# Optimization experiments

Hardware: AMD Instinct MI355X
Metric: run time of the kernel (lower is better)

The kernel has to match this reference:

```python
import jax, jax.numpy as jnp
import numpy as np

GROUP = 64  # quantization group size along the input dim


def dequantize(W_q, scale, zero):
    """int4 dequant: W_q uint8-packed [out, in/2] (two nibbles per byte),
    group-wise affine scale/zero [out, in/GROUP]. Returns float [out, in]."""
    out, half = W_q.shape
    hi = (W_q >> 4) & 0xF
    lo = W_q & 0xF
    w = jnp.stack([hi, lo], axis=-1).reshape(out, half * 2).astype(scale.dtype)
    w = w.reshape(out, -1, GROUP)  # [out, n_groups, GROUP]
    w = (w - zero[:, :, None]) * scale[:, :, None]
    return w.reshape(out, half * 2)


def setup_inputs() -> dict:
    key = jax.random.key(0)
    ks = jax.random.split(key, 10)
    hidden, inter = 4096, 11008
    B, S = 4, 1024
    x = jax.random.normal(ks[0], (B, S, hidden), dtype=jnp.float32)
    gate_Wq = jax.random.randint(ks[1], (inter, hidden // 2), 0, 256, dtype=jnp.int32)
    up_Wq = jax.random.randint(ks[2], (inter, hidden // 2), 0, 256, dtype=jnp.int32)
    down_Wq = jax.random.randint(ks[3], (hidden, inter // 2), 0, 256, dtype=jnp.int32)
    # small scales keep activations sane; zero points in [0, 15]
    gate_scale = jax.random.uniform(ks[4], (inter, hidden // GROUP)) * 0.01 + 1e-4
    gate_zero = jax.random.uniform(ks[5], (inter, hidden // GROUP)) * 15.0
    up_scale = jax.random.uniform(ks[6], (inter, hidden // GROUP)) * 0.01 + 1e-4
    up_zero = jax.random.uniform(ks[7], (inter, hidden // GROUP)) * 15.0
    down_scale = jax.random.uniform(ks[8], (hidden, inter // GROUP)) * 0.01 + 1e-4
    down_zero = jax.random.uniform(ks[9], (hidden, inter // GROUP)) * 15.0
    return {"x": x, "gate_Wq": gate_Wq, "up_Wq": up_Wq, "down_Wq": down_Wq,
            "gate_scale": gate_scale, "gate_zero": gate_zero,
            "up_scale": up_scale, "up_zero": up_zero,
            "down_scale": down_scale, "down_zero": down_zero}


def reference(x, gate_Wq, up_Wq, down_Wq, gate_scale, gate_zero,
              up_scale, up_zero, down_scale, down_zero):
    Wg = dequantize(gate_Wq, gate_scale, gate_zero)  # [inter, hidden]
    Wu = dequantize(up_Wq, up_scale, up_zero)        # [inter, hidden]
    Wd = dequantize(down_Wq, down_scale, down_zero)  # [hidden, inter]
    g = jnp.einsum('bsh,ih->bsi', x, Wg)
    u = jnp.einsum('bsh,ih->bsi', x, Wu)
    h = jax.nn.silu(g) * u
    return jnp.einsum('bsi,hi->bsh', h, Wd)
```

## Files before the change

### kernel.cpp

```cpp
#include <hip/hip_runtime.h>
#include <hip/hip_fp16.h>
#include <cstdint>
#include <cstddef>

#define HIDDEN 4096
#define INTER  11008
#define NTOK   4096
#define NG1    (HIDDEN/64)
#define NG2    (INTER/64)

typedef _Float16 f16;
typedef _Float16 f16x8 __attribute__((ext_vector_type(8)));
typedef float    f32x4 __attribute__((ext_vector_type(4)));

__device__ __forceinline__ void g2lds16(const void* g, void* l) {
  __builtin_amdgcn_global_load_lds(
      (const __attribute__((address_space(1))) uint32_t*)g,
      (__attribute__((address_space(3))) uint32_t*)l, 16, 0, 0);
}

__device__ __forceinline__ uint32_t dq2(uint32_t b, __half2 s2, __half2 nzs) {
  uint32_t qb = 0x64006400u | (b >> 4) | ((b & 0xFu) << 16);
  __half2 hq = __builtin_bit_cast(__half2, qb);
  __half2 t  = __hsub2(hq, __builtin_bit_cast(__half2, 0x64006400u));
  __half2 wv = __hfma2(t, s2, nzs);
  return __builtin_bit_cast(uint32_t, wv);
}

__global__ __launch_bounds__(256) void cvt_x(const float* __restrict__ x,
                                             f16* __restrict__ xh) {
  size_t i = ((size_t)blockIdx.x * 256 + threadIdx.x) * 8;
  float4 a = *(const float4*)(x + i);
  float4 b = *(const float4*)(x + i + 4);
  f16x8 o = {(f16)a.x, (f16)a.y, (f16)a.z, (f16)a.w,
             (f16)b.x, (f16)b.y, (f16)b.z, (f16)b.w};
  *(f16x8*)(xh + i) = o;
}

__global__ __launch_bounds__(512, 4) void gemm_gateup(
    const f16* __restrict__ xh,
    const uint32_t* __restrict__ gq, const uint32_t* __restrict__ uq,
    const float* __restrict__ gs, const float* __restrict__ gz,
    const float* __restrict__ us, const float* __restrict__ uz,
    f16* __restrict__ h) {
  extern __shared__ char smem[];
  f16* lA0 = (f16*)smem;
  f16* lA1 = (f16*)(smem + 32768);
  char* lBg = smem + 65536;
  char* lBu = smem + 73728;
  const int tid = threadIdx.x, lane = tid & 63, wave = tid >> 6;
  const int bm = blockIdx.x, bn = blockIdx.y;
  const int wm = wave >> 1, wn = wave & 1;

  const int arow0 = tid >> 3;
  const int ak8s  = (tid & 7) ^ (arow0 & 7);
  const f16* aptr = xh + (size_t)(bm * 256 + arow0) * HIDDEN + ak8s * 8;
  const int aoff = tid * 16;

  const int mat = tid >> 8;
  const int t = tid & 255;
  const int brow0 = t >> 3;
  const uint32_t* qp = (mat ? uq : gq) + (size_t)(bn * 64 + brow0) * (HIDDEN / 2) + (t & 7) * 4;
  const float* sp = (mat ? us : gs) + (size_t)(bn * 64 + brow0) * NG1;
  const float* zp = (mat ? uz : gz) + (size_t)(bn * 64 + brow0) * NG1;
  char* lb = mat ? lBu : lBg;
  const int bws0 = brow0 * 128 + (((t & 7) ^ (brow0 & 7)) << 4);

  int abase[4], asel[4];
#pragma unroll
  for (int im = 0; im < 4; ++im) {
    int r = wm * 64 + im * 16 + (lane & 15);
    abase[im] = r * 128; asel[im] = r & 7;
  }
  int bbase[2], bsel[2];
#pragma unroll
  for (int in_ = 0; in_ < 2; ++in_) {
    int r = wn * 32 + in_ * 16 + (lane & 15);
    bbase[in_] = r * 128; bsel[in_] = r & 7;
  }
  const int kchunk = lane >> 4;

  f32x4 accg[4][2] = {};
  f32x4 accu[4][2] = {};

  auto stageA = [&](const f16* src, f16* dst) {
#pragma unroll
    for (int i = 0; i < 4; ++i)
      g2lds16(src + (size_t)i * 64 * HIDDEN, (char*)dst + aoff + i * 8192);
  };
  auto loadB = [&](int ktn, uint4& w0, uint4& w1,
                   float& s0f, float& z0f, float& s1f, float& z1f) {
    w0 = *(const uint4*)(qp + (size_t)ktn * 32);
    w1 = *(const uint4*)(qp + (size_t)32 * (HIDDEN / 2) + (size_t)ktn * 32);
    s0f = sp[ktn]; z0f = zp[ktn];
    s1f = sp[32 * NG1 + ktn]; z1f = zp[32 * NG1 + ktn];
  };
  auto writeB = [&](uint4 w0, uint4 w1, float s0f, float z0f, float s1f, float z1f) {
    __half2 s0 = __float2half2_rn(s0f), n0 = __float2half2_rn(-z0f * s0f);
    __half2 s1 = __float2half2_rn(s1f), n1 = __float2half2_rn(-z1f * s1f);
    uint4 o0, o1;
    o0.x = dq2(w0.x, s0, n0); o0.y = dq2(w0.y, s0, n0);
    o0.z = dq2(w0.z, s0, n0); o0.w = dq2(w0.w, s0, n0);
    o1.x = dq2(w1.x, s1, n1); o1.y = dq2(w1.y, s1, n1);
    o1.z = dq2(w1.z, s1, n1); o1.w = dq2(w1.w, s1, n1);
    *(uint4*)(lb + bws0) = o0;
    *(uint4*)(lb + bws0 + 32 * 128) = o1;
  };
  auto compute = [&](const f16* lA) {
#pragma unroll
    for (int ks = 0; ks < 2; ++ks) {
      int kc = ks * 4 + kchunk;
      f16x8 a[4], bg[2], bu[2];
#pragma unroll
      for (int im = 0; im < 4; ++im)
        a[im] = *(const f16x8*)((const char*)lA + abase[im] + ((kc ^ asel[im]) << 4));
#pragma unroll
      for (int in_ = 0; in_ < 2; ++in_) {
        bg[in_] = *(const f16x8*)(lBg + bbase[in_] + ((kc ^ bsel[in_]) << 4));
        bu[in_] = *(const f16x8*)(lBu + bbase[in_] + ((kc ^ bsel[in_]) << 4));
      }
#pragma unroll
      for (int im = 0; im < 4; ++im)
#pragma unroll
        for (int in_ = 0; in_ < 2; ++in_) {
          accg[im][in_] = __builtin_amdgcn_mfma_f32_16x16x32_f16(a[im], bg[in_], accg[im][in_], 0, 0, 0);
          accu[im][in_] = __builtin_amdgcn_mfma_f32_16x16x32_f16(a[im], bu[in_], accu[im][in_], 0, 0, 0);
        }
    }
  };

  stageA(aptr, lA0);
  {
    uint4 w0, w1; float s0f, z0f, s1f, z1f;
    loadB(0, w0, w1, s0f, z0f, s1f, z1f);
    writeB(w0, w1, s0f, z0f, s1f, z1f);
  }
  __syncthreads();

  for (int kt = 0; kt < NG1 - 1; ++kt) {
    stageA(aptr + (size_t)(kt + 1) * 64, (kt & 1) ? lA0 : lA1);
    uint4 w0, w1; float s0f, z0f, s1f, z1f;
    loadB(kt + 1, w0, w1, s0f, z0f, s1f, z1f);
    compute((kt & 1) ? lA1 : lA0);
    __syncthreads();
    writeB(w0, w1, s0f, z0f, s1f, z1f);
    __syncthreads();
  }
  compute(((NG1 - 1) & 1) ? lA1 : lA0);

#pragma unroll
  for (int im = 0; im < 4; ++im)
#pragma unroll
    for (int in_ = 0; in_ < 2; ++in_)
#pragma unroll
      for (int r = 0; r < 4; ++r) {
        int row = bm * 256 + wm * 64 + im * 16 + (lane >> 4) * 4 + r;
        int col = bn * 64 + wn * 32 + in_ * 16 + (lane & 15);
        float g = accg[im][in_][r];
        float u = accu[im][in_][r];
        float hv = (g / (1.0f + __expf(-g))) * u;
        h[(size_t)row * INTER + col] = (f16)hv;
      }
}

__global__ __launch_bounds__(512, 4) void gemm_down(
    const f16* __restrict__ h, const uint32_t* __restrict__ dq_,
    const float* __restrict__ dsc, const float* __restrict__ dz,
    float* __restrict__ out) {
  extern __shared__ char smem[];
  f16* lA0 = (f16*)smem;
  f16* lA1 = (f16*)(smem + 32768);
  char* lB = smem + 65536;
  const int tid = threadIdx.x, lane = tid & 63, wave = tid >> 6;
  const int bm = blockIdx.x, bn = blockIdx.y;
  const int wm = wave >> 1, wn = wave & 1;

  const int arow0 = tid >> 3;
  const int ak8s  = (tid & 7) ^ (arow0 & 7);
  const f16* aptr = h + (size_t)(bm * 256 + arow0) * INTER + ak8s * 8;
  const int aoff = tid * 16;

  const int brow0 = tid >> 3;
  const uint32_t* qp = dq_ + (size_t)(bn * 128 + brow0) * (INTER / 2) + (tid & 7) * 4;
  const float* sp = dsc + (size_t)(bn * 128 + brow0) * NG2;
  const float* zp = dz + (size_t)(bn * 128 + brow0) * NG2;
  const int bws0 = brow0 * 128 + (((tid & 7) ^ (brow0 & 7)) << 4);

  int abase[4], asel[4];
#pragma unroll
  for (int im = 0; im < 4; ++im) {
    int r = wm * 64 + im * 16 + (lane & 15);
    abase[im] = r * 128; asel[im] = r & 7;
  }
  int bbase[4], bsel[4];
#pragma unroll
  for (int in_ = 0; in_ < 4; ++in_) {
    int r = wn * 64 + in_ * 16 + (lane & 15);
    bbase[in_] = r * 128; bsel[in_] = r & 7;
  }
  const int kchunk = lane >> 4;

  f32x4 acc[4][4] = {};

  auto stageA = [&](const f16* src, f16* dst) {
#pragma unroll
    for (int i = 0; i < 4; ++i)
      g2lds16(src + (size_t)i * 64 * INTER, (char*)dst + aoff + i * 8192);
  };
  auto loadB = [&](int ktn, uint4& w0, uint4& w1,
                   float& s0f, float& z0f, float& s1f, float& z1f) {
    w0 = *(const uint4*)(qp + (size_t)ktn * 32);
    w1 = *(const uint4*)(qp + (size_t)64 * (INTER / 2) + (size_t)ktn * 32);
    s0f = sp[ktn]; z0f = zp[ktn];
    s1f = sp[64 * NG2 + ktn]; z1f = zp[64 * NG2 + ktn];
  };
  auto writeB = [&](uint4 w0, uint4 w1, float s0f, float z0f, float s1f, float z1f) {
    __half2 s0 = __float2half2_rn(s0f), n0 = __float2half2_rn(-z0f * s0f);
    __half2 s1 = __float2half2_rn(s1f), n1 = __float2half2_rn(-z1f * s1f);
    uint4 o0, o1;
    o0.x = dq2(w0.x, s0, n0); o0.y = dq2(w0.y, s0, n0);
    o0.z = dq2(w0.z, s0, n0); o0.w = dq2(w0.w, s0, n0);
    o1.x = dq2(w1.x, s1, n1); o1.y = dq2(w1.y, s1, n1);
    o1.z = dq2(w1.z, s1, n1); o1.w = dq2(w1.w, s1, n1);
    *(uint4*)(lB + bws0) = o0;
    *(uint4*)(lB + bws0 + 64 * 128) = o1;
  };
  auto compute = [&](const f16* lA) {
#pragma unroll
    for (int ks = 0; ks < 2; ++ks) {
      int kc = ks * 4 + kchunk;
      f16x8 a[4], b[4];
#pragma unroll
      for (int im = 0; im < 4; ++im)
        a[im] = *(const f16x8*)((const char*)lA + abase[im] + ((kc ^ asel[im]) << 4));
#pragma unroll
      for (int in_ = 0; in_ < 4; ++in_)
        b[in_] = *(const f16x8*)(lB + bbase[in_] + ((kc ^ bsel[in_]) << 4));
#pragma unroll
      for (int im = 0; im < 4; ++im)
#pragma unroll
        for (int in_ = 0; in_ < 4; ++in_)
          acc[im][in_] = __builtin_amdgcn_mfma_f32_16x16x32_f16(a[im], b[in_], acc[im][in_], 0, 0, 0);
    }
  };

  stageA(aptr, lA0);
  {
    uint4 w0, w1; float s0f, z0f, s1f, z1f;
    loadB(0, w0, w1, s0f, z0f, s1f, z1f);
    writeB(w0, w1, s0f, z0f, s1f, z1f);
  }
  __syncthreads();

  for (int kt = 0; kt < NG2 - 1; ++kt) {
    stageA(aptr + (size_t)(kt + 1) * 64, (kt & 1) ? lA0 : lA1);
    uint4 w0, w1; float s0f, z0f, s1f, z1f;
    loadB(kt + 1, w0, w1, s0f, z0f, s1f, z1f);
    compute((kt & 1) ? lA1 : lA0);
    __syncthreads();
    writeB(w0, w1, s0f, z0f, s1f, z1f);
    __syncthreads();
  }
  compute(((NG2 - 1) & 1) ? lA1 : lA0);

#pragma unroll
  for (int im = 0; im < 4; ++im)
#pragma unroll
    for (int in_ = 0; in_ < 4; ++in_)
#pragma unroll
      for (int r = 0; r < 4; ++r) {
        int row = bm * 256 + wm * 64 + im * 16 + (lane >> 4) * 4 + r;
        int col = bn * 128 + wn * 64 + in_ * 16 + (lane & 15);
        out[(size_t)row * HIDDEN + col] = acc[im][in_][r];
      }
}

extern "C" void kernel_launch(void* const* d_in, const int* in_sizes, int n_in,
                              void* d_out, int out_size, void* d_ws, size_t ws_size,
                              hipStream_t stream) {
  const float*    x   = (const float*)d_in[0];
  const uint32_t* gq  = (const uint32_t*)d_in[1];
  const uint32_t* uq  = (const uint32_t*)d_in[2];
  const uint32_t* dqw = (const uint32_t*)d_in[3];
  const float*    gs  = (const float*)d_in[4];
  const float*    gz  = (const float*)d_in[5];
  const float*    us  = (const float*)d_in[6];
  const float*    uz  = (const float*)d_in[7];
  const float*    dsc = (const float*)d_in[8];
  const float*    dzz = (const float*)d_in[9];

  f16* xh   = (f16*)d_ws;
  f16* hbuf = (f16*)((char*)d_ws + (size_t)NTOK * HIDDEN * 2);
  float* out = (float*)d_out;

  const int LDS_BYTES = 80 * 1024;
  (void)hipFuncSetAttribute((const void*)gemm_gateup,
                            hipFuncAttributeMaxDynamicSharedMemorySize, LDS_BYTES);
  (void)hipFuncSetAttribute((const void*)gemm_down,
                            hipFuncAttributeMaxDynamicSharedMemorySize, LDS_BYTES);

  cvt_x<<<dim3((NTOK * HIDDEN) / (256 * 8)), 256, 0, stream>>>(x, xh);
  gemm_gateup<<<dim3(NTOK / 256, INTER / 64), 512, LDS_BYTES, stream>>>(
      xh, gq, uq, gs, gz, us, uz, hbuf);
  gemm_down<<<dim3(NTOK / 256, HIDDEN / 128), 512, LDS_BYTES, stream>>>(
      hbuf, dqw, dsc, dzz, out);
}
```

Baseline: 1.502 ms.

## Register-prefetch A and B, double-buffer dequantized B in LDS, prioritize MFMA

Replaces direct global-to-LDS A staging with register loads written into a single LDS A buffer, and double-buffers the dequantized B tile so the next tile's dequant write overlaps the current compute. Raw B data is prefetched two steps ahead, MFMA sections are raised with s_setprio, and barriers wait only on LDS counters. LDS drops to 64KB. The cost is more VGPR pressure and exposed global-load latency before the A write.

```diff
diff --git a/kernel.cpp b/kernel.cpp
--- a/kernel.cpp
+++ b/kernel.cpp
@@ -13,10 +13,10 @@
 typedef _Float16 f16x8 __attribute__((ext_vector_type(8)));
 typedef float    f32x4 __attribute__((ext_vector_type(4)));
 
-__device__ __forceinline__ void g2lds16(const void* g, void* l) {
-  __builtin_amdgcn_global_load_lds(
-      (const __attribute__((address_space(1))) uint32_t*)g,
-      (__attribute__((address_space(3))) uint32_t*)l, 16, 0, 0);
+__device__ __forceinline__ void wg_barrier_lgkm() {
+  asm volatile("s_waitcnt lgkmcnt(0)" ::: "memory");
+  __builtin_amdgcn_s_barrier();
+  asm volatile("" ::: "memory");
 }
 
 __device__ __forceinline__ uint32_t dq2(uint32_t b, __half2 s2, __half2 nzs) {
@@ -26,6 +26,8 @@
   __half2 wv = __hfma2(t, s2, nzs);
   return __builtin_bit_cast(uint32_t, wv);
 }
+
+struct Bp { uint4 w0, w1; float s0, z0, s1, z1; };
 
 __global__ __launch_bounds__(256) void cvt_x(const float* __restrict__ x,
                                              f16* __restrict__ xh) {
@@ -44,10 +46,9 @@
     const float* __restrict__ us, const float* __restrict__ uz,
     f16* __restrict__ h) {
   extern __shared__ char smem[];
-  f16* lA0 = (f16*)smem;
-  f16* lA1 = (f16*)(smem + 32768);
-  char* lBg = smem + 65536;
-  char* lBu = smem + 73728;
+  f16* lA = (f16*)smem;
+  char* lBgBase = smem + 32768;
+  char* lBuBase = smem + 49152;
   const int tid = threadIdx.x, lane = tid & 63, wave = tid >> 6;
   const int bm = blockIdx.x, bn = blockIdx.y;
   const int wm = wave >> 1, wn = wave & 1;
@@ -63,7 +64,7 @@
   const uint32_t* qp = (mat ? uq : gq) + (size_t)(bn * 64 + brow0) * (HIDDEN / 2) + (t & 7) * 4;
   const float* sp = (mat ? us : gs) + (size_t)(bn * 64 + brow0) * NG1;
   const float* zp = (mat ? uz : gz) + (size_t)(bn * 64 + brow0) * NG1;
-  char* lb = mat ? lBu : lBg;
+  char* lbBase = mat ? lBuBase : lBgBase;
   const int bws0 = brow0 * 128 + (((t & 7) ^ (brow0 & 7)) << 4);
 
   int abase[4], asel[4];
@@ -83,30 +84,38 @@
   f32x4 accg[4][2] = {};
   f32x4 accu[4][2] = {};
 
-  auto stageA = [&](const f16* src, f16* dst) {
+  uint4 ar[4];
+  auto loadA = [&](int kt) {
 #pragma unroll
     for (int i = 0; i < 4; ++i)
-      g2lds16(src + (size_t)i * 64 * HIDDEN, (char*)dst + aoff + i * 8192);
-  };
-  auto loadB = [&](int ktn, uint4& w0, uint4& w1,
-                   float& s0f, float& z0f, float& s1f, float& z1f) {
-    w0 = *(const uint4*)(qp + (size_t)ktn * 32);
-    w1 = *(const uint4*)(qp + (size_t)32 * (HIDDEN / 2) + (size_t)ktn * 32);
-    s0f = sp[ktn]; z0f = zp[ktn];
-    s1f = sp[32 * NG1 + ktn]; z1f = zp[32 * NG1 + ktn];
-  };
-  auto writeB = [&](uint4 w0, uint4 w1, float s0f, float z0f, float s1f, float z1f) {
-    __half2 s0 = __float2half2_rn(s0f), n0 = __float2half2_rn(-z0f * s0f);
-    __half2 s1 = __float2half2_rn(s1f), n1 = __float2half2_rn(-z1f * s1f);
+      ar[i] = *(const uint4*)(aptr + (size_t)kt * 64 + (size_t)i * 64 * HIDDEN);
+  };
+  auto writeA = [&]() {
+#pragma unroll
+    for (int i = 0; i < 4; ++i)
+      *(uint4*)((char*)lA + aoff + i * 8192) = ar[i];
+  };
+  auto loadB = [&](int ktn, Bp& r) {
+    r.w0 = *(const uint4*)(qp + (size_t)ktn * 32);
+    r.w1 = *(const uint4*)(qp + (size_t)32 * (HIDDEN / 2) + (size_t)ktn * 32);
+    r.s0 = sp[ktn]; r.z0 = zp[ktn];
+    r.s1 = sp[32 * NG1 + ktn]; r.z1 = zp[32 * NG1 + ktn];
+  };
+  auto writeB = [&](const Bp& r, int pb) {
+    char* lb = lbBase + pb * 8192;
+    __half2 s0 = __float2half2_rn(r.s0), n0 = __float2half2_rn(-r.z0 * r.s0);
+    __half2 s1 = __float2half2_rn(r.s1), n1 = __float2half2_rn(-r.z1 * r.s1);
     uint4 o0, o1;
-    o0.x = dq2(w0.x, s0, n0); o0.y = dq2(w0.y, s0, n0);
-    o0.z = dq2(w0.z, s0, n0); o0.w = dq2(w0.w, s0, n0);
-    o1.x = dq2(w1.x, s1, n1); o1.y = dq2(w1.y, s1, n1);
-    o1.z = dq2(w1.z, s1, n1); o1.w = dq2(w1.w, s1, n1);
+    o0.x = dq2(r.w0.x, s0, n0); o0.y = dq2(r.w0.y, s0, n0);
+    o0.z = dq2(r.w0.z, s0, n0); o0.w = dq2(r.w0.w, s0, n0);
+    o1.x = dq2(r.w1.x, s1, n1); o1.y = dq2(r.w1.y, s1, n1);
+    o1.z = dq2(r.w1.z, s1, n1); o1.w = dq2(r.w1.w, s1, n1);
     *(uint4*)(lb + bws0) = o0;
     *(uint4*)(lb + bws0 + 32 * 128) = o1;
   };
-  auto compute = [&](const f16* lA) {
+  auto compute = [&](int cb) {
+    const char* bg0 = lBgBase + cb * 8192;
+    const char* bu0 = lBuBase + cb * 8192;
 #pragma unroll
     for (int ks = 0; ks < 2; ++ks) {
       int kc = ks * 4 + kchunk;
@@ -116,9 +125,10 @@
         a[im] = *(const f16x8*)((const char*)lA + abase[im] + ((kc ^ asel[im]) << 4));
 #pragma unroll
       for (int in_ = 0; in_ < 2; ++in_) {
-        bg[in_] = *(const f16x8*)(lBg + bbase[in_] + ((kc ^ bsel[in_]) << 4));
-        bu[in_] = *(const f16x8*)(lBu + bbase[in_] + ((kc ^ bsel[in_]) << 4));
+        bg[in_] = *(const f16x8*)(bg0 + bbase[in_] + ((kc ^ bsel[in_]) << 4));
+        bu[in_] = *(const f16x8*)(bu0 + bbase[in_] + ((kc ^ bsel[in_]) << 4));
       }
+      __builtin_amdgcn_s_setprio(1);
 #pragma unroll
       for (int im = 0; im < 4; ++im)
 #pragma unroll
@@ -126,27 +136,30 @@
           accg[im][in_] = __builtin_amdgcn_mfma_f32_16x16x32_f16(a[im], bg[in_], accg[im][in_], 0, 0, 0);
           accu[im][in_] = __builtin_amdgcn_mfma_f32_16x16x32_f16(a[im], bu[in_], accu[im][in_], 0, 0, 0);
         }
+      __builtin_amdgcn_s_setprio(0);
     }
   };
 
-  stageA(aptr, lA0);
-  {
-    uint4 w0, w1; float s0f, z0f, s1f, z1f;
-    loadB(0, w0, w1, s0f, z0f, s1f, z1f);
-    writeB(w0, w1, s0f, z0f, s1f, z1f);
-  }
-  __syncthreads();
+  loadA(0);
+  Bp br0, brc, brn;
+  loadB(0, br0);
+  loadB(1, brc);
+  writeA();
+  writeB(br0, 0);
+  wg_barrier_lgkm();
 
   for (int kt = 0; kt < NG1 - 1; ++kt) {
-    stageA(aptr + (size_t)(kt + 1) * 64, (kt & 1) ? lA0 : lA1);
-    uint4 w0, w1; float s0f, z0f, s1f, z1f;
-    loadB(kt + 1, w0, w1, s0f, z0f, s1f, z1f);
-    compute((kt & 1) ? lA1 : lA0);
-    __syncthreads();
-    writeB(w0, w1, s0f, z0f, s1f, z1f);
-    __syncthreads();
-  }
-  compute(((NG1 - 1) & 1) ? lA1 : lA0);
+    loadA(kt + 1);
+    loadB(kt + 2 < NG1 ? kt + 2 : NG1 - 1, brn);
+    __builtin_amdgcn_sched_barrier(0);
+    writeB(brc, (kt + 1) & 1);
+    compute(kt & 1);
+    wg_barrier_lgkm();
+    writeA();
+    wg_barrier_lgkm();
+    brc = brn;
+  }
+  compute((NG1 - 1) & 1);
 
 #pragma unroll
   for (int im = 0; im < 4; ++im)
@@ -168,9 +181,8 @@
     const float* __restrict__ dsc, const float* __restrict__ dz,
     float* __restrict__ out) {
   extern __shared__ char smem[];
-  f16* lA0 = (f16*)smem;
-  f16* lA1 = (f16*)(smem + 32768);
-  char* lB = smem + 65536;
+  f16* lA = (f16*)smem;
+  char* lBBase = smem + 32768;
   const int tid = threadIdx.x, lane = tid & 63, wave = tid >> 6;
   const int bm = blockIdx.x, bn = blockIdx.y;
   const int wm = wave >> 1, wn = wave & 1;
@@ -202,30 +214,37 @@
 
   f32x4 acc[4][4] = {};
 
-  auto stageA = [&](const f16* src, f16* dst) {
+  uint4 ar[4];
+  auto loadA = [&](int kt) {
 #pragma unroll
     for (int i = 0; i < 4; ++i)
-      g2lds16(src + (size_t)i * 64 * INTER, (char*)dst + aoff + i * 8192);
-  };
-  auto loadB = [&](int ktn, uint4& w0, uint4& w1,
-                   float& s0f, float& z0f, float& s1f, float& z1f) {
-    w0 = *(const uint4*)(qp + (size_t)ktn * 32);
-    w1 = *(const uint4*)(qp + (size_t)64 * (INTER / 2) + (size_t)ktn * 32);
-    s0f = sp[ktn]; z0f = zp[ktn];
-    s1f = sp[64 * NG2 + ktn]; z1f = zp[64 * NG2 + ktn];
-  };
-  auto writeB = [&](uint4 w0, uint4 w1, float s0f, float z0f, float s1f, float z1f) {
-    __half2 s0 = __float2half2_rn(s0f), n0 = __float2half2_rn(-z0f * s0f);
-    __half2 s1 = __float2half2_rn(s1f), n1 = __float2half2_rn(-z1f * s1f);
+      ar[i] = *(const uint4*)(aptr + (size_t)kt * 64 + (size_t)i * 64 * INTER);
+  };
+  auto writeA = [&]() {
+#pragma unroll
+    for (int i = 0; i < 4; ++i)
+      *(uint4*)((char*)lA + aoff + i * 8192) = ar[i];
+  };
+  auto loadB = [&](int ktn, Bp& r) {
+    r.w0 = *(const uint4*)(qp + (size_t)ktn * 32);
+    r.w1 = *(const uint4*)(qp + (size_t)64 * (INTER / 2) + (size_t)ktn * 32);
+    r.s0 = sp[ktn]; r.z0 = zp[ktn];
+    r.s1 = sp[64 * NG2 + ktn]; r.z1 = zp[64 * NG2 + ktn];
+  };
+  auto writeB = [&](const Bp& r, int pb) {
+    char* lb = lBBase + pb * 16384;
+    __half2 s0 = __float2half2_rn(r.s0), n0 = __float2half2_rn(-r.z0 * r.s0);
+    __half2 s1 = __float2half2_rn(r.s1), n1 = __float2half2_rn(-r.z1 * r.s1);
     uint4 o0, o1;
-    o0.x = dq2(w0.x, s0, n0); o0.y = dq2(w0.y, s0, n0);
-    o0.z = dq2(w0.z, s0, n0); o0.w = dq2(w0.w, s0, n0);
-    o1.x = dq2(w1.x, s1, n1); o1.y = dq2(w1.y, s1, n1);
-    o1.z = dq2(w1.z, s1, n1); o1.w = dq2(w1.w, s1, n1);
-    *(uint4*)(lB + bws0) = o0;
-    *(uint4*)(lB + bws0 + 64 * 128) = o1;
-  };
-  auto compute = [&](const f16* lA) {
+    o0.x = dq2(r.w0.x, s0, n0); o0.y = dq2(r.w0.y, s0, n0);
+    o0.z = dq2(r.w0.z, s0, n0); o0.w = dq2(r.w0.w, s0, n0);
+    o1.x = dq2(r.w1.x, s1, n1); o1.y = dq2(r.w1.y, s1, n1);
+    o1.z = dq2(r.w1.z, s1, n1); o1.w = dq2(r.w1.w, s1, n1);
+    *(uint4*)(lb + bws0) = o0;
+    *(uint4*)(lb + bws0 + 64 * 128) = o1;
+  };
+  auto compute = [&](int cb) {
+    const char* lb0 = lBBase + cb * 16384;
 #pragma unroll
     for (int ks = 0; ks < 2; ++ks) {
       int kc = ks * 4 + kchunk;
@@ -235,33 +254,37 @@
         a[im] = *(const f16x8*)((const char*)lA + abase[im] + ((kc ^ asel[im]) << 4));
 #pragma unroll
       for (int in_ = 0; in_ < 4; ++in_)
-        b[in_] = *(const f16x8*)(lB + bbase[in_] + ((kc ^ bsel[in_]) << 4));
+        b[in_] = *(const f16x8*)(lb0 + bbase[in_] + ((kc ^ bsel[in_]) << 4));
+      __builtin_amdgcn_s_setprio(1);
 #pragma unroll
       for (int im = 0; im < 4; ++im)
 #pragma unroll
         for (int in_ = 0; in_ < 4; ++in_)
           acc[im][in_] = __builtin_amdgcn_mfma_f32_16x16x32_f16(a[im], b[in_], acc[im][in_], 0, 0, 0);
+      __builtin_amdgcn_s_setprio(0);
     }
   };
 
-  stageA(aptr, lA0);
-  {
-    uint4 w0, w1; float s0f, z0f, s1f, z1f;
-    loadB(0, w0, w1, s0f, z0f, s1f, z1f);
-    writeB(w0, w1, s0f, z0f, s1f, z1f);
-  }
-  __syncthreads();
+  loadA(0);
+  Bp br0, brc, brn;
+  loadB(0, br0);
+  loadB(1, brc);
+  writeA();
+  writeB(br0, 0);
+  wg_barrier_lgkm();
 
   for (int kt = 0; kt < NG2 - 1; ++kt) {
-    stageA(aptr + (size_t)(kt + 1) * 64, (kt & 1) ? lA0 : lA1);
-    uint4 w0, w1; float s0f, z0f, s1f, z1f;
-    loadB(kt + 1, w0, w1, s0f, z0f, s1f, z1f);
-    compute((kt & 1) ? lA1 : lA0);
-    __syncthreads();
-    writeB(w0, w1, s0f, z0f, s1f, z1f);
-    __syncthreads();
-  }
-  compute(((NG2 - 1) & 1) ? lA1 : lA0);
+    loadA(kt + 1);
+    loadB(kt + 2 < NG2 ? kt + 2 : NG2 - 1, brn);
+    __builtin_amdgcn_sched_barrier(0);
+    writeB(brc, (kt + 1) & 1);
+    compute(kt & 1);
+    wg_barrier_lgkm();
+    writeA();
+    wg_barrier_lgkm();
+    brc = brn;
+  }
+  compute((NG2 - 1) & 1);
 
 #pragma unroll
   for (int im = 0; im < 4; ++im)
@@ -293,7 +316,7 @@
   f16* hbuf = (f16*)((char*)d_ws + (size_t)NTOK * HIDDEN * 2);
   float* out = (float*)d_out;
 
-  const int LDS_BYTES = 80 * 1024;
+  const int LDS_BYTES = 64 * 1024;
   (void)hipFuncSetAttribute((const void*)gemm_gateup,
                             hipFuncAttributeMaxDynamicSharedMemorySize, LDS_BYTES);
   (void)hipFuncSetAttribute((const void*)gemm_down,
```

New measurement: 3.990 ms. 2.66x slower.

## Pre-dequantize int4 weights to fp16 in workspace before plain fp16 GEMMs

Applied to the files above, without the earlier changes.

Adds a dequant kernel that expands each int4 weight matrix into fp16 in workspace once per call. The GEMMs then read fp16 B tiles directly instead of dequantizing inside the main loop, which takes the dequant ALU work out of the MFMA loop. Block indices are also remapped so neighbouring blocks share data in cache. The cost is extra HBM traffic to write and reread the fp16 weights, and the new path needs enough workspace, otherwise it falls back to the old kernels.

```diff
diff --git a/kernel.cpp b/kernel.cpp
--- a/kernel.cpp
+++ b/kernel.cpp
@@ -37,7 +37,240 @@
   *(f16x8*)(xh + i) = o;
 }
 
-__global__ __launch_bounds__(512, 4) void gemm_gateup(
+__global__ __launch_bounds__(256) void deq_w(const uint32_t* __restrict__ q,
+                                             const float* __restrict__ s,
+                                             const float* __restrict__ z,
+                                             f16* __restrict__ out) {
+  int g = blockIdx.x * 256 + threadIdx.x;
+  const uint32_t* qp = q + (size_t)g * 32;
+  float sf = s[g], zf = z[g];
+  __half2 s2 = __float2half2_rn(sf), nzs = __float2half2_rn(-zf * sf);
+  f16* op = out + (size_t)g * 64;
+#pragma unroll
+  for (int i = 0; i < 8; ++i) {
+    uint4 w = *(const uint4*)(qp + i * 4);
+    uint4 o;
+    o.x = dq2(w.x, s2, nzs); o.y = dq2(w.y, s2, nzs);
+    o.z = dq2(w.z, s2, nzs); o.w = dq2(w.w, s2, nzs);
+    *(uint4*)(op + i * 8) = o;
+  }
+}
+
+__global__ __launch_bounds__(512, 4) void gemm_gateup_f(
+    const f16* __restrict__ xh, const f16* __restrict__ wg,
+    const f16* __restrict__ wu, f16* __restrict__ h) {
+  extern __shared__ char smem[];
+  f16* lA0 = (f16*)smem;
+  f16* lA1 = (f16*)(smem + 32768);
+  char* lBg = smem + 65536;
+  char* lBu = smem + 73728;
+  const int tid = threadIdx.x, lane = tid & 63, wave = tid >> 6;
+  const int bid = blockIdx.y * 16 + blockIdx.x;
+  const int sw  = (bid & 7) * 344 + (bid >> 3);
+  const int bm = sw & 15, bn = sw >> 4;
+  const int wm = wave >> 1, wn = wave & 1;
+
+  const int arow0 = tid >> 3;
+  const int ak8s  = (tid & 7) ^ (arow0 & 7);
+  const f16* aptr = xh + (size_t)(bm * 256 + arow0) * HIDDEN + ak8s * 8;
+  const int aoff = tid * 16;
+
+  const int mat = tid >> 8;
+  const int t = tid & 255;
+  const int brow0 = t >> 3;
+  const f16* bp = (mat ? wu : wg) + (size_t)(bn * 64 + brow0) * HIDDEN + (t & 7) * 8;
+  char* lb = mat ? lBu : lBg;
+  const int bws0 = brow0 * 128 + (((t & 7) ^ (brow0 & 7)) << 4);
+
+  int abase[4], asel[4];
+#pragma unroll
+  for (int im = 0; im < 4; ++im) {
+    int r = wm * 64 + im * 16 + (lane & 15);
+    abase[im] = r * 128; asel[im] = r & 7;
+  }
+  int bbase[2], bsel[2];
+#pragma unroll
+  for (int in_ = 0; in_ < 2; ++in_) {
+    int r = wn * 32 + in_ * 16 + (lane & 15);
+    bbase[in_] = r * 128; bsel[in_] = r & 7;
+  }
+  const int kchunk = lane >> 4;
+
+  f32x4 accg[4][2] = {};
+  f32x4 accu[4][2] = {};
+
+  auto stageA = [&](const f16* src, f16* dst) {
+#pragma unroll
+    for (int i = 0; i < 4; ++i)
+      g2lds16(src + (size_t)i * 64 * HIDDEN, (char*)dst + aoff + i * 8192);
+  };
+  auto loadB = [&](int ktn, uint4& w0, uint4& w1) {
+    w0 = *(const uint4*)(bp + (size_t)ktn * 64);
+    w1 = *(const uint4*)(bp + (size_t)32 * HIDDEN + (size_t)ktn * 64);
+  };
+  auto writeB = [&](uint4 w0, uint4 w1) {
+    *(uint4*)(lb + bws0) = w0;
+    *(uint4*)(lb + bws0 + 32 * 128) = w1;
+  };
+  auto compute = [&](const f16* lA) {
+#pragma unroll
+    for (int ks = 0; ks < 2; ++ks) {
+      int kc = ks * 4 + kchunk;
+      f16x8 a[4], bg[2], bu[2];
+#pragma unroll
+      for (int im = 0; im < 4; ++im)
+        a[im] = *(const f16x8*)((const char*)lA + abase[im] + ((kc ^ asel[im]) << 4));
+#pragma unroll
+      for (int in_ = 0; in_ < 2; ++in_) {
+        bg[in_] = *(const f16x8*)(lBg + bbase[in_] + ((kc ^ bsel[in_]) << 4));
+        bu[in_] = *(const f16x8*)(lBu + bbase[in_] + ((kc ^ bsel[in_]) << 4));
+      }
+#pragma unroll
+      for (int im = 0; im < 4; ++im)
+#pragma unroll
+        for (int in_ = 0; in_ < 2; ++in_) {
+          accg[im][in_] = __builtin_amdgcn_mfma_f32_16x16x32_f16(a[im], bg[in_], accg[im][in_], 0, 0, 0);
+          accu[im][in_] = __builtin_amdgcn_mfma_f32_16x16x32_f16(a[im], bu[in_], accu[im][in_], 0, 0, 0);
+        }
+    }
+  };
+
+  stageA(aptr, lA0);
+  {
+    uint4 w0, w1;
+    loadB(0, w0, w1);
+    writeB(w0, w1);
+  }
+  __syncthreads();
+
+  for (int kt = 0; kt < NG1 - 1; ++kt) {
+    stageA(aptr + (size_t)(kt + 1) * 64, (kt & 1) ? lA0 : lA1);
+    uint4 w0, w1;
+    loadB(kt + 1, w0, w1);
+    compute((kt & 1) ? lA1 : lA0);
+    __syncthreads();
+    writeB(w0, w1);
+    __syncthreads();
+  }
+  compute(((NG1 - 1) & 1) ? lA1 : lA0);
+
+#pragma unroll
+  for (int im = 0; im < 4; ++im)
+#pragma unroll
+    for (int in_ = 0; in_ < 2; ++in_)
+#pragma unroll
+      for (int r = 0; r < 4; ++r) {
+        int row = bm * 256 + wm * 64 + im * 16 + (lane >> 4) * 4 + r;
+        int col = bn * 64 + wn * 32 + in_ * 16 + (lane & 15);
+        float g = accg[im][in_][r];
+        float u = accu[im][in_][r];
+        float hv = (g / (1.0f + __expf(-g))) * u;
+        h[(size_t)row * INTER + col] = (f16)hv;
+      }
+}
+
+__global__ __launch_bounds__(512, 4) void gemm_down_f(
+    const f16* __restrict__ h, const f16* __restrict__ wd,
+    float* __restrict__ out) {
+  extern __shared__ char smem[];
+  f16* lA0 = (f16*)smem;
+  f16* lA1 = (f16*)(smem + 32768);
+  char* lB = smem + 65536;
+  const int tid = threadIdx.x, lane = tid & 63, wave = tid >> 6;
+  const int bid = blockIdx.y * 16 + blockIdx.x;
+  const int sw  = (bid & 7) * 64 + (bid >> 3);
+  const int bm = sw & 15, bn = sw >> 4;
+  const int wm = wave >> 1, wn = wave & 1;
+
+  const int arow0 = tid >> 3;
+  const int ak8s  = (tid & 7) ^ (arow0 & 7);
+  const f16* aptr = h + (size_t)(bm * 256 + arow0) * INTER + ak8s * 8;
+  const int aoff = tid * 16;
+
+  const int brow0 = tid >> 3;
+  const f16* bp = wd + (size_t)(bn * 128 + brow0) * INTER + (tid & 7) * 8;
+  const int bws0 = brow0 * 128 + (((tid & 7) ^ (brow0 & 7)) << 4);
+
+  int abase[4], asel[4];
+#pragma unroll
+  for (int im = 0; im < 4; ++im) {
+    int r = wm * 64 + im * 16 + (lane & 15);
+    abase[im] = r * 128; asel[im] = r & 7;
+  }
+  int bbase[4], bsel[4];
+#pragma unroll
+  for (int in_ = 0; in_ < 4; ++in_) {
+    int r = wn * 64 + in_ * 16 + (lane & 15);
+    bbase[in_] = r * 128; bsel[in_] = r & 7;
+  }
+  const int kchunk = lane >> 4;
+
+  f32x4 acc[4][4] = {};
+
+  auto stageA = [&](const f16* src, f16* dst) {
+#pragma unroll
+    for (int i = 0; i < 4; ++i)
+      g2lds16(src + (size_t)i * 64 * INTER, (char*)dst + aoff + i * 8192);
+  };
+  auto loadB = [&](int ktn, uint4& w0, uint4& w1) {
+    w0 = *(const uint4*)(bp + (size_t)ktn * 64);
+    w1 = *(const uint4*)(bp + (size_t)64 * INTER + (size_t)ktn * 64);
+  };
+  auto writeB = [&](uint4 w0, uint4 w1) {
+    *(uint4*)(lB + bws0) = w0;
+    *(uint4*)(lB + bws0 + 64 * 128) = w1;
+  };
+  auto compute = [&](const f16* lA) {
+#pragma unroll
+    for (int ks = 0; ks < 2; ++ks) {
+      int kc = ks * 4 + kchunk;
+      f16x8 a[4], b[4];
+#pragma unroll
+      for (int im = 0; im < 4; ++im)
+        a[im] = *(const f16x8*)((const char*)lA + abase[im] + ((kc ^ asel[im]) << 4));
+#pragma unroll
+      for (int in_ = 0; in_ < 4; ++in_)
+        b[in_] = *(const f16x8*)(lB + bbase[in_] + ((kc ^ bsel[in_]) << 4));
+#pragma unroll
+      for (int im = 0; im < 4; ++im)
+#pragma unroll
+        for (int in_ = 0; in_ < 4; ++in_)
+          acc[im][in_] = __builtin_amdgcn_mfma_f32_16x16x32_f16(a[im], b[in_], acc[im][in_], 0, 0, 0);
+    }
+  };
+
+  stageA(aptr, lA0);
+  {
+    uint4 w0, w1;
+    loadB(0, w0, w1);
+    writeB(w0, w1);
+  }
+  __syncthreads();
+
+  for (int kt = 0; kt < NG2 - 1; ++kt) {
+    stageA(aptr + (size_t)(kt + 1) * 64, (kt & 1) ? lA0 : lA1);
+    uint4 w0, w1;
+    loadB(kt + 1, w0, w1);
+    compute((kt & 1) ? lA1 : lA0);
+    __syncthreads();
+    writeB(w0, w1);
+    __syncthreads();
+  }
+  compute(((NG2 - 1) & 1) ? lA1 : lA0);
+
+#pragma unroll
+  for (int im = 0; im < 4; ++im)
+#pragma unroll
+    for (int in_ = 0; in_ < 4; ++in_)
+#pragma unroll
+      for (int r = 0; r < 4; ++r) {
+        int row = bm * 256 + wm * 64 + im * 16 + (lane >> 4) * 4 + r;
+        int col = bn * 128 + wn * 64 + in_ * 16 + (lane & 15);
+        out[(size_t)row * HIDDEN + col] = acc[im][in_][r];
+      }
+}
+
+__global__ __launch_bounds__(512, 4) void gemm_gateup_q(
     const f16* __restrict__ xh,
     const uint32_t* __restrict__ gq, const uint32_t* __restrict__ uq,
     const float* __restrict__ gs, const float* __restrict__ gz,
@@ -163,7 +396,7 @@
       }
 }
 
-__global__ __launch_bounds__(512, 4) void gemm_down(
+__global__ __launch_bounds__(512, 4) void gemm_down_q(
     const f16* __restrict__ h, const uint32_t* __restrict__ dq_,
     const float* __restrict__ dsc, const float* __restrict__ dz,
     float* __restrict__ out) {
@@ -289,19 +522,39 @@
   const float*    dsc = (const float*)d_in[8];
   const float*    dzz = (const float*)d_in[9];
 
+  const size_t XH = (size_t)NTOK * HIDDEN * 2;
+  const size_t HB = (size_t)NTOK * INTER * 2;
+  const size_t WB = (size_t)INTER * HIDDEN * 2;
   f16* xh   = (f16*)d_ws;
-  f16* hbuf = (f16*)((char*)d_ws + (size_t)NTOK * HIDDEN * 2);
+  f16* hbuf = (f16*)((char*)d_ws + XH);
   float* out = (float*)d_out;
 
   const int LDS_BYTES = 80 * 1024;
-  (void)hipFuncSetAttribute((const void*)gemm_gateup,
-                            hipFuncAttributeMaxDynamicSharedMemorySize, LDS_BYTES);
-  (void)hipFuncSetAttribute((const void*)gemm_down,
-                            hipFuncAttributeMaxDynamicSharedMemorySize, LDS_BYTES);
 
   cvt_x<<<dim3((NTOK * HIDDEN) / (256 * 8)), 256, 0, stream>>>(x, xh);
-  gemm_gateup<<<dim3(NTOK / 256, INTER / 64), 512, LDS_BYTES, stream>>>(
-      xh, gq, uq, gs, gz, us, uz, hbuf);
-  gemm_down<<<dim3(NTOK / 256, HIDDEN / 128), 512, LDS_BYTES, stream>>>(
-      hbuf, dqw, dsc, dzz, out);
-}
+
+  if (ws_size >= XH + HB + 2 * WB) {
+    f16* W1 = (f16*)((char*)d_ws + XH + HB);
+    f16* W2 = (f16*)((char*)d_ws + XH + HB + WB);
+    (void)hipFuncSetAttribute((const void*)gemm_gateup_f,
+                              hipFuncAttributeMaxDynamicSharedMemorySize, LDS_BYTES);
+    (void)hipFuncSetAttribute((const void*)gemm_down_f,
+                              hipFuncAttributeMaxDynamicSharedMemorySize, LDS_BYTES);
+    deq_w<<<dim3((INTER * NG1) / 256), 256, 0, stream>>>(gq, gs, gz, W1);
+    deq_w<<<dim3((INTER * NG1) / 256), 256, 0, stream>>>(uq, us, uz, W2);
+    gemm_gateup_f<<<dim3(NTOK / 256, INTER / 64), 512, LDS_BYTES, stream>>>(
+        xh, W1, W2, hbuf);
+    deq_w<<<dim3((HIDDEN * NG2) / 256), 256, 0, stream>>>(dqw, dsc, dzz, W1);
+    gemm_down_f<<<dim3(NTOK / 256, HIDDEN / 128), 512, LDS_BYTES, stream>>>(
+        hbuf, W1, out);
+  } else {
+    (void)hipFuncSetAttribute((const void*)gemm_gateup_q,
+                              hipFuncAttributeMaxDynamicSharedMemorySize, LDS_BYTES);
+    (void)hipFuncSetAttribute((const void*)gemm_down_q,
+                              hipFuncAttributeMaxDynamicSharedMemorySize, LDS_BYTES);
+    gemm_gateup_q<<<dim3(NTOK / 256, INTER / 64), 512, LDS_BYTES, stream>>>(
+        xh, gq, uq, gs, gz, us, uz, hbuf);
+    gemm_down_q<<<dim3(NTOK / 256, HIDDEN / 128), 512, LDS_BYTES, stream>>>(
+        hbuf, dqw, dsc, dzz, out);
+  }
+}
```

After: 1.536 ms. +2.3%, slower.

## Pre-dequantize weights to fp16 and use larger-tile plain fp16 GEMMs

Applied to the files above, without the earlier changes.

Adds a separate dequantization kernel that expands the int4 weights into fp16 buffers in workspace. Gate/up and down projections then run as plain fp16 GEMMs with 256x128 (and 256x256) tiles, so dequantization no longer happens inside the GEMM inner loops and each weight is dequantized once instead of once per M-tile. SiLU and the product are combined through an LDS exchange between waves. The cost is extra weight memory traffic, more workspace, and 128KB of LDS per block. The old fused kernels are kept as a fallback when the workspace is too small.

```diff
diff --git a/kernel.cpp b/kernel.cpp
--- a/kernel.cpp
+++ b/kernel.cpp
@@ -37,7 +37,221 @@
   *(f16x8*)(xh + i) = o;
 }
 
-__global__ __launch_bounds__(512, 4) void gemm_gateup(
+__global__ __launch_bounds__(256) void deq_w(const uint32_t* __restrict__ q,
+                                             const float* __restrict__ s,
+                                             const float* __restrict__ z,
+                                             f16* __restrict__ out) {
+  int g = blockIdx.x * 256 + threadIdx.x;
+  const uint32_t* qp = q + (size_t)g * 32;
+  float sf = s[g], zf = z[g];
+  __half2 s2 = __float2half2_rn(sf), nzs = __float2half2_rn(-zf * sf);
+  f16* op = out + (size_t)g * 64;
+#pragma unroll
+  for (int i = 0; i < 8; ++i) {
+    uint4 w = *(const uint4*)(qp + i * 4);
+    uint4 o;
+    o.x = dq2(w.x, s2, nzs); o.y = dq2(w.y, s2, nzs);
+    o.z = dq2(w.z, s2, nzs); o.w = dq2(w.w, s2, nzs);
+    *(uint4*)(op + i * 8) = o;
+  }
+}
+
+
+__global__ __launch_bounds__(512, 2) void gemm_gateup2(
+    const f16* __restrict__ xh, const f16* __restrict__ wg,
+    const f16* __restrict__ wu, f16* __restrict__ h) {
+  extern __shared__ char smem[];
+  const int tid = threadIdx.x, lane = tid & 63, wave = tid >> 6;
+  const int bm = blockIdx.x, bn = blockIdx.y;
+  const int wm = wave >> 2, wn = wave & 3;
+
+  const int srow = tid >> 3;
+  const int sk8  = (tid & 7) ^ (srow & 7);
+  const f16* aptr = xh + (size_t)(bm * 256 + srow) * HIDDEN + sk8 * 8;
+  const f16* gptr = wg + (size_t)(bn * 128 + srow) * HIDDEN + sk8 * 8;
+  const f16* uptr = wu + (size_t)(bn * 128 + srow) * HIDDEN + sk8 * 8;
+  const int soff = tid * 16;
+
+  int abase[8], asel[8];
+#pragma unroll
+  for (int im = 0; im < 8; ++im) {
+    int r = wm * 128 + im * 16 + (lane & 15);
+    abase[im] = r * 128; asel[im] = r & 7;
+  }
+  int bbase[4], bsel[4];
+#pragma unroll
+  for (int in_ = 0; in_ < 4; ++in_) {
+    int r = wn * 64 + in_ * 16 + (lane & 15);
+    bbase[in_] = 32768 + r * 128; bsel[in_] = r & 7;
+  }
+  const int kchunk = lane >> 4;
+
+  f32x4 acc[8][4] = {};
+
+  auto stage = [&](int kt, int pb) {
+    char* base = smem + pb * 65536;
+    const f16* ap = aptr + (size_t)kt * 64;
+#pragma unroll
+    for (int i = 0; i < 4; ++i)
+      g2lds16(ap + (size_t)i * 64 * HIDDEN, base + soff + i * 8192);
+    const f16* gp = gptr + (size_t)kt * 64;
+    g2lds16(gp,                           base + 32768 + soff);
+    g2lds16(gp + (size_t)64 * HIDDEN,     base + 32768 + soff + 8192);
+    const f16* up = uptr + (size_t)kt * 64;
+    g2lds16(up,                           base + 32768 + soff + 16384);
+    g2lds16(up + (size_t)64 * HIDDEN,     base + 32768 + soff + 24576);
+  };
+  auto compute = [&](int pb) {
+    const char* base = smem + pb * 65536;
+#pragma unroll
+    for (int ks = 0; ks < 2; ++ks) {
+      int kc = ks * 4 + kchunk;
+      f16x8 a[8], b[4];
+#pragma unroll
+      for (int im = 0; im < 8; ++im)
+        a[im] = *(const f16x8*)(base + abase[im] + ((kc ^ asel[im]) << 4));
+#pragma unroll
+      for (int in_ = 0; in_ < 4; ++in_)
+        b[in_] = *(const f16x8*)(base + bbase[in_] + ((kc ^ bsel[in_]) << 4));
+#pragma unroll
+      for (int im = 0; im < 8; ++im)
+#pragma unroll
+        for (int in_ = 0; in_ < 4; ++in_)
+          acc[im][in_] = __builtin_amdgcn_mfma_f32_16x16x32_f16(a[im], b[in_], acc[im][in_], 0, 0, 0);
+    }
+  };
+
+  stage(0, 0);
+  __syncthreads();
+
+  for (int kt = 0; kt < NG1 - 1; ++kt) {
+    stage(kt + 1, (kt + 1) & 1);
+    __builtin_amdgcn_sched_barrier(0);
+    compute(kt & 1);
+    __syncthreads();
+  }
+  compute((NG1 - 1) & 1);
+
+  const int r0 = (lane >> 4) * 4;
+  const int c0 = lane & 15;
+  if (wn < 2) {
+    char* reg = smem + (wm * 2 + wn) * 16384;
+#pragma unroll
+    for (int im = 0; im < 8; ++im)
+#pragma unroll
+      for (int in_ = 0; in_ < 4; ++in_)
+#pragma unroll
+        for (int r = 0; r < 4; ++r) {
+          float g = acc[im][in_][r];
+          float sg = g / (1.0f + __expf(-g));
+          int rowL = im * 16 + r0 + r, colL = in_ * 16 + c0;
+          *(f16*)(reg + rowL * 128 + colL * 2) = (f16)sg;
+        }
+  }
+  __syncthreads();
+  if (wn >= 2) {
+    const char* reg = smem + (wm * 2 + (wn - 2)) * 16384;
+#pragma unroll
+    for (int im = 0; im < 8; ++im)
+#pragma unroll
+      for (int in_ = 0; in_ < 4; ++in_)
+#pragma unroll
+        for (int r = 0; r < 4; ++r) {
+          int rowL = im * 16 + r0 + r, colL = in_ * 16 + c0;
+          float sg = (float)*(const f16*)(reg + rowL * 128 + colL * 2);
+          float hv = sg * acc[im][in_][r];
+          int row = bm * 256 + wm * 128 + rowL;
+          int col = bn * 128 + (wn - 2) * 64 + colL;
+          h[(size_t)row * INTER + col] = (f16)hv;
+        }
+  }
+}
+
+__global__ __launch_bounds__(512, 2) void gemm_down2(
+    const f16* __restrict__ h, const f16* __restrict__ wd,
+    float* __restrict__ out) {
+  extern __shared__ char smem[];
+  const int tid = threadIdx.x, lane = tid & 63, wave = tid >> 6;
+  const int bm = blockIdx.x, bn = blockIdx.y;
+  const int wm = wave >> 2, wn = wave & 3;
+
+  const int srow = tid >> 3;
+  const int sk8  = (tid & 7) ^ (srow & 7);
+  const f16* aptr = h  + (size_t)(bm * 256 + srow) * INTER + sk8 * 8;
+  const f16* bptr = wd + (size_t)(bn * 256 + srow) * INTER + sk8 * 8;
+  const int soff = tid * 16;
+
+  int abase[8], asel[8];
+#pragma unroll
+  for (int im = 0; im < 8; ++im) {
+    int r = wm * 128 + im * 16 + (lane & 15);
+    abase[im] = r * 128; asel[im] = r & 7;
+  }
+  int bbase[4], bsel[4];
+#pragma unroll
+  for (int in_ = 0; in_ < 4; ++in_) {
+    int r = wn * 64 + in_ * 16 + (lane & 15);
+    bbase[in_] = 32768 + r * 128; bsel[in_] = r & 7;
+  }
+  const int kchunk = lane >> 4;
+
+  f32x4 acc[8][4] = {};
+
+  auto stage = [&](int kt, int pb) {
+    char* base = smem + pb * 65536;
+    const f16* ap = aptr + (size_t)kt * 64;
+    const f16* bp = bptr + (size_t)kt * 64;
+#pragma unroll
+    for (int i = 0; i < 4; ++i) {
+      g2lds16(ap + (size_t)i * 64 * INTER, base + soff + i * 8192);
+      g2lds16(bp + (size_t)i * 64 * INTER, base + 32768 + soff + i * 8192);
+    }
+  };
+  auto compute = [&](int pb) {
+    const char* base = smem + pb * 65536;
+#pragma unroll
+    for (int ks = 0; ks < 2; ++ks) {
+      int kc = ks * 4 + kchunk;
+      f16x8 a[8], b[4];
+#pragma unroll
+      for (int im = 0; im < 8; ++im)
+        a[im] = *(const f16x8*)(base + abase[im] + ((kc ^ asel[im]) << 4));
+#pragma unroll
+      for (int in_ = 0; in_ < 4; ++in_)
+        b[in_] = *(const f16x8*)(base + bbase[in_] + ((kc ^ bsel[in_]) << 4));
+#pragma unroll
+      for (int im = 0; im < 8; ++im)
+#pragma unroll
+        for (int in_ = 0; in_ < 4; ++in_)
+          acc[im][in_] = __builtin_amdgcn_mfma_f32_16x16x32_f16(a[im], b[in_], acc[im][in_], 0, 0, 0);
+    }
+  };
+
+  stage(0, 0);
+  __syncthreads();
+  for (int kt = 0; kt < NG2 - 1; ++kt) {
+    stage(kt + 1, (kt + 1) & 1);
+    __builtin_amdgcn_sched_barrier(0);
+    compute(kt & 1);
+    __syncthreads();
+  }
+  compute((NG2 - 1) & 1);
+
+  const int r0 = (lane >> 4) * 4;
+  const int c0 = lane & 15;
+#pragma unroll
+  for (int im = 0; im < 8; ++im)
+#pragma unroll
+    for (int in_ = 0; in_ < 4; ++in_)
+#pragma unroll
+      for (int r = 0; r < 4; ++r) {
+        int row = bm * 256 + wm * 128 + im * 16 + r0 + r;
+        int col = bn * 256 + wn * 64 + in_ * 16 + c0;
+        out[(size_t)row * HIDDEN + col] = acc[im][in_][r];
+      }
+}
+
+__global__ __launch_bounds__(512, 4) void gemm_gateup_q(
     const f16* __restrict__ xh,
     const uint32_t* __restrict__ gq, const uint32_t* __restrict__ uq,
     const float* __restrict__ gs, const float* __restrict__ gz,
@@ -163,7 +377,7 @@
       }
 }
 
-__global__ __launch_bounds__(512, 4) void gemm_down(
+__global__ __launch_bounds__(512, 4) void gemm_down_q(
     const f16* __restrict__ h, const uint32_t* __restrict__ dq_,
     const float* __restrict__ dsc, const float* __restrict__ dz,
     float* __restrict__ out) {
@@ -289,19 +503,39 @@
   const float*    dsc = (const float*)d_in[8];
   const float*    dzz = (const float*)d_in[9];
 
+  const size_t XH = (size_t)NTOK * HIDDEN * 2;
+  const size_t HB = (size_t)NTOK * INTER * 2;
+  const size_t WB = (size_t)INTER * HIDDEN * 2;
   f16* xh   = (f16*)d_ws;
-  f16* hbuf = (f16*)((char*)d_ws + (size_t)NTOK * HIDDEN * 2);
+  f16* hbuf = (f16*)((char*)d_ws + XH);
   float* out = (float*)d_out;
 
-  const int LDS_BYTES = 80 * 1024;
-  (void)hipFuncSetAttribute((const void*)gemm_gateup,
-                            hipFuncAttributeMaxDynamicSharedMemorySize, LDS_BYTES);
-  (void)hipFuncSetAttribute((const void*)gemm_down,
-                            hipFuncAttributeMaxDynamicSharedMemorySize, LDS_BYTES);
-
   cvt_x<<<dim3((NTOK * HIDDEN) / (256 * 8)), 256, 0, stream>>>(x, xh);
-  gemm_gateup<<<dim3(NTOK / 256, INTER / 64), 512, LDS_BYTES, stream>>>(
-      xh, gq, uq, gs, gz, us, uz, hbuf);
-  gemm_down<<<dim3(NTOK / 256, HIDDEN / 128), 512, LDS_BYTES, stream>>>(
-      hbuf, dqw, dsc, dzz, out);
-}
+
+  if (ws_size >= XH + HB + 2 * WB) {
+    f16* W1 = (f16*)((char*)d_ws + XH + HB);
+    f16* W2 = (f16*)((char*)d_ws + XH + HB + WB);
+    const int LDS_BIG = 128 * 1024;
+    (void)hipFuncSetAttribute((const void*)gemm_gateup2,
+                              hipFuncAttributeMaxDynamicSharedMemorySize, LDS_BIG);
+    (void)hipFuncSetAttribute((const void*)gemm_down2,
+                              hipFuncAttributeMaxDynamicSharedMemorySize, LDS_BIG);
+    deq_w<<<dim3((INTER * NG1) / 256), 256, 0, stream>>>(gq, gs, gz, W1);
+    deq_w<<<dim3((INTER * NG1) / 256), 256, 0, stream>>>(uq, us, uz, W2);
+    gemm_gateup2<<<dim3(NTOK / 256, INTER / 128), 512, LDS_BIG, stream>>>(
+        xh, W1, W2, hbuf);
+    deq_w<<<dim3((HIDDEN * NG2) / 256), 256, 0, stream>>>(dqw, dsc, dzz, W1);
+    gemm_down2<<<dim3(NTOK / 256, HIDDEN / 256), 512, LDS_BIG, stream>>>(
+        hbuf, W1, out);
+  } else {
+    const int LDS_Q = 80 * 1024;
+    (void)hipFuncSetAttribute((const void*)gemm_gateup_q,
+                              hipFuncAttributeMaxDynamicSharedMemorySize, LDS_Q);
+    (void)hipFuncSetAttribute((const void*)gemm_down_q,
+                              hipFuncAttributeMaxDynamicSharedMemorySize, LDS_Q);
+    gemm_gateup_q<<<dim3(NTOK / 256, INTER / 64), 512, LDS_Q, stream>>>(
+        xh, gq, uq, gs, gz, us, uz, hbuf);
+    gemm_down_q<<<dim3(NTOK / 256, HIDDEN / 128), 512, LDS_Q, stream>>>(
+        hbuf, dqw, dsc, dzz, out);
+  }
+}
```

Measured after the change: 1.446 ms. -3.7%, faster.
